# Kernel optimization log

Hardware: AMD Instinct MI355X
Metric: run time of the kernel (lower is better)

Reference implementation:

```python
import jax, jax.numpy as jnp
import numpy as np

N = 50000   # nodes
E = 800000  # edges
NF = 16     # num_node_features
EF = 8      # num_edge_features
H = 4       # heads
C = 64      # out_channels per head
NC = 4      # num_classes


def setup_inputs() -> dict:
    key = jax.random.key(0)
    ks = jax.random.split(key, 32)
    w = lambda k, shape: (jax.random.normal(k, shape, jnp.float32) * 0.05)
    inp = {
        "x": jax.random.normal(ks[0], (N, NF), jnp.float32),
        "edge_index": jax.random.randint(ks[1], (2, E), 0, N, dtype=jnp.int32),
        "edge_attr": jax.random.normal(ks[2], (E, EF), jnp.float32),
        # fc00
        "w00": w(ks[3], (NF, 64)), "b00": jnp.zeros((64,), jnp.float32),
        # edge MLP
        "we1": w(ks[4], (EF, 64)), "be1": jnp.zeros((64,), jnp.float32),
        "we2": w(ks[5], (64, 64)), "be2": jnp.zeros((64,), jnp.float32),
        "we3": w(ks[6], (64, 64)), "be3": jnp.zeros((64,), jnp.float32),
        # TransformerConv projections (64 -> H*C = 256)
        "wq": w(ks[7], (64, H * C)), "bq": jnp.zeros((H * C,), jnp.float32),
        "wk": w(ks[8], (64, H * C)), "bk": jnp.zeros((H * C,), jnp.float32),
        "wv": w(ks[9], (64, H * C)), "bv": jnp.zeros((H * C,), jnp.float32),
        "wedge": w(ks[10], (64, H * C)), "bedge": jnp.zeros((H * C,), jnp.float32),
        "wskip": w(ks[11], (64, H * C)), "bskip": jnp.zeros((H * C,), jnp.float32),
        # LayerNorm(256)
        "ln_g": jnp.ones((H * C,), jnp.float32), "ln_b": jnp.zeros((H * C,), jnp.float32),
        # head
        "w1": w(ks[12], (H * C, 128)), "b1": jnp.zeros((128,), jnp.float32),
        "w2": w(ks[13], (128, NC)), "b2": jnp.zeros((NC,), jnp.float32),
    }
    return inp


def _forward(x, edge_attr, w00, b00, we1, be1, we2, be2, we3, be3,
             wq, bq, wk, bk, wv, bv, wedge, bedge, wskip, bskip,
             ln_g, ln_b, w1, b1, w2, b2, edge_index):
    relu = jax.nn.relu
    n = x.shape[0]
    # node embed (dropout = identity in eval)
    x1 = relu(x @ w00 + b00)                              # [N, 64]
    # edge MLP
    e = relu(edge_attr @ we1 + be1)
    e = relu(e @ we2 + be2)
    e = relu(e @ we3 + be3)                               # [E, 64]
    src, dst = edge_index[0], edge_index[1]
    # project nodes once, then gather per edge
    q = (x1 @ wq + bq).reshape(n, H, C)[dst]              # [E, H, C]
    k = (x1 @ wk + bk).reshape(n, H, C)[src]
    v = (x1 @ wv + bv).reshape(n, H, C)[src]
    eh = (e @ wedge + bedge).reshape(-1, H, C)            # [E, H, C]
    k = k + eh
    v = v + eh
    alpha = jnp.sum(q * k, axis=-1) / np.sqrt(C)          # [E, H]
    # segment softmax over incoming edges of each target node
    m = jax.ops.segment_max(alpha, dst, num_segments=n)   # [N, H]
    m = jnp.where(jnp.isfinite(m), m, 0.0)
    p = jnp.exp(alpha - m[dst])
    s = jax.ops.segment_sum(p, dst, num_segments=n)
    a = p / (s[dst] + 1e-16)                              # [E, H]
    out = jax.ops.segment_sum(v * a[:, :, None], dst, num_segments=n)
    out = out.reshape(n, H * C) + (x1 @ wskip + bskip)    # root skip (root_weight=True)
    # LayerNorm(256)
    mu = jnp.mean(out, axis=-1, keepdims=True)
    var = jnp.mean(jnp.square(out - mu), axis=-1, keepdims=True)
    out = (out - mu) * jax.lax.rsqrt(var + 1e-5) * ln_g + ln_b
    out = relu(out)
    h = relu(out @ w1 + b1)
    logits = h @ w2 + b2
    return jax.nn.log_softmax(logits, axis=1)


def reference(x, edge_index, edge_attr, w00, b00, we1, be1, we2, be2, we3, be3,
              wq, bq, wk, bk, wv, bv, wedge, bedge, wskip, bskip,
              ln_g, ln_b, w1, b1, w2, b2):
    return _forward(x, edge_attr, w00, b00, we1, be1, we2, be2, we3, be3,
                    wq, bq, wk, bk, wv, bv, wedge, bedge, wskip, bskip,
                    ln_g, ln_b, w1, b1, w2, b2, edge_index)
```

## Files before the change

kernel.cpp:

```cpp
#include <hip/hip_runtime.h>
#include <hip/hip_bf16.h>

typedef unsigned short u16;
typedef __attribute__((ext_vector_type(8))) short bf16x8;
typedef __attribute__((ext_vector_type(4))) float f32x4;

#define NN 50000
#define NE 800000
#define SCAN_NB ((NN + 255) / 256)

__device__ __forceinline__ float bf2f(u16 u) { return __uint_as_float(((unsigned)u) << 16); }
__device__ __forceinline__ u16 f2bf(float f) {
  unsigned u = __float_as_uint(f);
  return (u16)((u + 0x7FFFu + ((u >> 16) & 1u)) >> 16);
}

__global__ void k_zero(int* __restrict__ deg) {
  int i = blockIdx.x * 256 + threadIdx.x;
  if (i < NN) deg[i] = 0;
}

__global__ void k_hist(const int* __restrict__ ei, int* __restrict__ deg) {
  int i = blockIdx.x * 256 + threadIdx.x;
  if (i < NE) {
    int d = ei[NE + i];
    if (d >= 0 && d < NN) atomicAdd(&deg[d], 1);
  }
}

__global__ __launch_bounds__(256) void k_scan_a(const int* __restrict__ deg,
                                                int* __restrict__ bsum) {
  __shared__ int red[256];
  const int t = threadIdx.x;
  const int i = blockIdx.x * 256 + t;
  red[t] = (i < NN) ? deg[i] : 0;
  __syncthreads();
  #pragma unroll
  for (int s = 128; s > 0; s >>= 1) {
    if (t < s) red[t] += red[t + s];
    __syncthreads();
  }
  if (t == 0) bsum[blockIdx.x] = red[0];
}

__global__ __launch_bounds__(256) void k_scan_b(const int* __restrict__ bsum,
                                                int* __restrict__ boff,
                                                int* __restrict__ rowptr) {
  __shared__ int s[256];
  const int t = threadIdx.x;
  int v = (t < SCAN_NB) ? bsum[t] : 0;
  s[t] = v;
  __syncthreads();
  #pragma unroll
  for (int o = 1; o < 256; o <<= 1) {
    int u = (t >= o) ? s[t - o] : 0;
    __syncthreads();
    s[t] += u;
    __syncthreads();
  }
  if (t < SCAN_NB) boff[t] = s[t] - v;
  if (t == 255) rowptr[NN] = s[255];
}

__global__ __launch_bounds__(256) void k_scan_c(const int* __restrict__ deg,
                                                const int* __restrict__ boff,
                                                int* __restrict__ rowptr,
                                                int* __restrict__ cursor) {
  __shared__ int s[256];
  const int t = threadIdx.x;
  const int i = blockIdx.x * 256 + t;
  int v = (i < NN) ? deg[i] : 0;
  s[t] = v;
  __syncthreads();
  #pragma unroll
  for (int o = 1; o < 256; o <<= 1) {
    int u = (t >= o) ? s[t - o] : 0;
    __syncthreads();
    s[t] += u;
    __syncthreads();
  }
  if (i < NN) {
    int r = boff[blockIdx.x] + s[t] - v;
    rowptr[i] = r;
    cursor[i] = r;
  }
}

__global__ void k_scatter(const int* __restrict__ ei, int* __restrict__ cursor,
                          int* __restrict__ slist, int* __restrict__ e2p) {
  int i = blockIdx.x * 256 + threadIdx.x;
  if (i < NE) {
    int d = ei[NE + i];
    if (d >= 0 && d < NN) {
      int pos = atomicAdd(&cursor[d], 1);
      if (pos >= 0 && pos < NE) {
        e2p[i] = pos;
        int s = ei[i];
        slist[pos] = max(0, min(s, NN - 1));
      }
    }
  }
}

__global__ void k_prep_ng(const float* __restrict__ w00, const float* __restrict__ wq,
                          const float* __restrict__ wedge, const float* __restrict__ wk,
                          u16* __restrict__ wB00t, u16* __restrict__ wqt, u16* __restrict__ BGQ) {
  int i = blockIdx.x * 256 + threadIdx.x;
  if (i < 2048) {
    int n = i >> 5, k = i & 31;
    wB00t[i] = (k < 16) ? f2bf(w00[k * 64 + n]) : (u16)0;
  } else if (i < 2048 + 16384) {
    int i2 = i - 2048;
    int n = i2 >> 6, k = i2 & 63;
    wqt[i2] = f2bf(wq[k * 256 + n]);
  } else if (i < 2048 + 16384 + 131072) {
    int i2 = i - 2048 - 16384;
    int col = i2 >> 8, k = i2 & 255;
    float v;
    if (col < 256) v = ((k >> 6) == (col >> 6)) ? wedge[(col & 63) * 256 + k] : 0.f;
    else { int c = col - 256; v = ((k >> 6) == (c >> 6)) ? wk[(c & 63) * 256 + k] : 0.f; }
    BGQ[i2] = f2bf(v);
  }
}

__global__ void k_prep_w(const float* __restrict__ we1, const float* __restrict__ we2,
                         const float* __restrict__ we3,
                         u16* __restrict__ wB1t, u16* __restrict__ wB2t, u16* __restrict__ wB3t) {
  int i = blockIdx.x * 256 + threadIdx.x;
  if (i < 512) {
    int n = i >> 3, k = i & 7;
    wB1t[i] = f2bf(we1[k * 64 + n]);
  } else if (i < 512 + 4096) {
    int i2 = i - 512;
    int n = i2 >> 6, k = i2 & 63;
    wB2t[i2] = f2bf(we2[k * 64 + n]);
  } else if (i < 512 + 8192) {
    int i2 = i - 512 - 4096;
    int n = i2 >> 6, k = i2 & 63;
    wB3t[i2] = f2bf(we3[k * 64 + n]);
  }
}

__global__ void k_prep_b(const float* __restrict__ wedge, const float* __restrict__ wv,
                         const float* __restrict__ wskip, u16* __restrict__ Bt) {
  const int col = blockIdx.x;
  const int k = threadIdx.x;
  float v;
  if (k < 256) v = ((k >> 6) == (col >> 6)) ? wedge[(k & 63) * 256 + col] : 0.f;
  else if (k < 512) { int k2 = k - 256; v = ((k2 >> 6) == (col >> 6)) ? wv[(k2 & 63) * 256 + col] : 0.f; }
  else v = wskip[(k - 512) * 256 + col];
  Bt[col * 576 + k] = f2bf(v);
}

__global__ void k_prep_h(const float* __restrict__ w1, u16* __restrict__ Bt1) {
  const int col = blockIdx.x;
  const int k = threadIdx.x;
  Bt1[col * 256 + k] = f2bf(w1[k * 128 + col]);
}

__global__ __launch_bounds__(256) void k_ng(
    const float* __restrict__ x, const u16* __restrict__ wB00t, const float* __restrict__ b00,
    const u16* __restrict__ wqt, const float* __restrict__ bq,
    const u16* __restrict__ BGQ,
    u16* __restrict__ x1g, u16* __restrict__ Gg, u16* __restrict__ Qkg) {
  __shared__ u16 xs[64 * 32];
  __shared__ u16 x1s[64 * 72];
  __shared__ u16 qs[64 * 264];
  const int t = threadIdx.x;
  const int w = t >> 6, l = t & 63;
  const int quad = l >> 4, li = l & 15;
  const int n0 = blockIdx.x * 64;
  const f32x4 zc = {0.f, 0.f, 0.f, 0.f};

  for (int q = t; q < 2048; q += 256) {
    int row = q >> 5, k = q & 31;
    float v = (k < 16 && n0 + row < NN) ? x[(size_t)(n0 + row) * 16 + k] : 0.f;
    xs[row * 32 + k] = f2bf(v);
  }
  __syncthreads();

  {
    bf16x8 bf = *(const bf16x8*)(wB00t + (w * 16 + li) * 32 + quad * 8);
    float bc = b00[w * 16 + li];
    #pragma unroll
    for (int mt = 0; mt < 4; ++mt) {
      bf16x8 af = *(const bf16x8*)(xs + (mt * 16 + li) * 32 + quad * 8);
      f32x4 d = __builtin_amdgcn_mfma_f32_16x16x32_bf16(af, bf, zc, 0, 0, 0);
      #pragma unroll
      for (int r = 0; r < 4; ++r)
        x1s[(mt * 16 + quad * 4 + r) * 72 + w * 16 + li] = f2bf(fmaxf(d[r] + bc, 0.f));
    }
  }
  __syncthreads();

  #pragma unroll
  for (int it = 0; it < 2; ++it) {
    int i = (it * 256 + t) * 8;
    int row = i >> 6, col = i & 63;
    if (n0 + row < NN)
      *(uint4*)(x1g + (size_t)(n0 + row) * 64 + col) = *(const uint4*)(x1s + row * 72 + col);
  }

  {
    f32x4 acc[4][4];
    #pragma unroll
    for (int mt = 0; mt < 4; ++mt)
      #pragma unroll
      for (int nt = 0; nt < 4; ++nt) acc[mt][nt] = zc;
    const int colbase = w * 64;
    #pragma unroll
    for (int s = 0; s < 2; ++s) {
      bf16x8 bf[4];
      #pragma unroll
      for (int nt = 0; nt < 4; ++nt)
        bf[nt] = *(const bf16x8*)(wqt + (size_t)(colbase + nt * 16 + li) * 64 + s * 32 + quad * 8);
      #pragma unroll
      for (int mt = 0; mt < 4; ++mt) {
        bf16x8 af = *(const bf16x8*)(x1s + (mt * 16 + li) * 72 + s * 32 + quad * 8);
        #pragma unroll
        for (int nt = 0; nt < 4; ++nt)
          acc[mt][nt] = __builtin_amdgcn_mfma_f32_16x16x32_bf16(af, bf[nt], acc[mt][nt], 0, 0, 0);
      }
    }
    float bqc[4];
    #pragma unroll
    for (int nt = 0; nt < 4; ++nt) bqc[nt] = bq[colbase + nt * 16 + li];
    #pragma unroll
    for (int mt = 0; mt < 4; ++mt)
      #pragma unroll
      for (int nt = 0; nt < 4; ++nt)
        #pragma unroll
        for (int r = 0; r < 4; ++r)
          qs[(mt * 16 + quad * 4 + r) * 264 + colbase + nt * 16 + li] = f2bf(acc[mt][nt][r] + bqc[nt]);
  }
  __syncthreads();

  #pragma unroll
  for (int half = 0; half < 2; ++half) {
    f32x4 acc[4][4];
    #pragma unroll
    for (int mt = 0; mt < 4; ++mt)
      #pragma unroll
      for (int nt = 0; nt < 4; ++nt) acc[mt][nt] = zc;
    const int colbase = w * 64;
    const size_t bofs = (size_t)(half * 256) * 256;
    #pragma unroll
    for (int s = 0; s < 8; ++s) {
      bf16x8 bf[4];
      #pragma unroll
      for (int nt = 0; nt < 4; ++nt)
        bf[nt] = *(const bf16x8*)(BGQ + bofs + (size_t)(colbase + nt * 16 + li) * 256 + s * 32 + quad * 8);
      #pragma unroll
      for (int mt = 0; mt < 4; ++mt) {
        bf16x8 af = *(const bf16x8*)(qs + (mt * 16 + li) * 264 + s * 32 + quad * 8);
        #pragma unroll
        for (int nt = 0; nt < 4; ++nt)
          acc[mt][nt] = __builtin_amdgcn_mfma_f32_16x16x32_bf16(af, bf[nt], acc[mt][nt], 0, 0, 0);
      }
    }
    u16* dst = half ? Qkg : Gg;
    #pragma unroll
    for (int mt = 0; mt < 4; ++mt)
      #pragma unroll
      for (int r = 0; r < 4; ++r) {
        int node = n0 + mt * 16 + quad * 4 + r;
        if (node < NN) {
          #pragma unroll
          for (int nt = 0; nt < 4; ++nt)
            dst[(size_t)node * 256 + colbase + nt * 16 + li] = f2bf(acc[mt][nt][r]);
        }
      }
  }
}

#define EPB 128
#define APAD 72
__global__ __launch_bounds__(256) void k_edge_mlp(
    const float* __restrict__ ea,
    const u16* __restrict__ wB1t, const u16* __restrict__ wB2t, const u16* __restrict__ wB3t,
    const float* __restrict__ be1, const float* __restrict__ be2, const float* __restrict__ be3,
    const int* __restrict__ e2p, u16* __restrict__ e3g) {
  __shared__ u16 actA[EPB * APAD];
  __shared__ u16 actB[EPB * APAD];
  const int t = threadIdx.x;
  const int w = t >> 6, l = t & 63;
  const int quad = l >> 4, li = l & 15;
  const int e0 = blockIdx.x * EPB;
  const f32x4 zc = {0.f, 0.f, 0.f, 0.f};

  float b1c[4], b2c[4], b3c[4];
  #pragma unroll
  for (int nt = 0; nt < 4; ++nt) {
    b1c[nt] = be1[nt * 16 + li];
    b2c[nt] = be2[nt * 16 + li];
    b3c[nt] = be3[nt * 16 + li];
  }

  bf16x8 b1f[4];
  #pragma unroll
  for (int nt = 0; nt < 4; ++nt) {
    bf16x8 z = {};
    if (quad == 0) z = *(const bf16x8*)(wB1t + (nt * 16 + li) * 8);
    b1f[nt] = z;
  }
  #pragma unroll
  for (int mi = 0; mi < 2; ++mi) {
    const int mt = w * 2 + mi;
    bf16x8 af = {};
    if (quad == 0) {
      const float4* pa = (const float4*)(ea + (size_t)(e0 + mt * 16 + li) * 8);
      float4 p0 = pa[0], p1 = pa[1];
      af[0] = (short)f2bf(p0.x); af[1] = (short)f2bf(p0.y);
      af[2] = (short)f2bf(p0.z); af[3] = (short)f2bf(p0.w);
      af[4] = (short)f2bf(p1.x); af[5] = (short)f2bf(p1.y);
      af[6] = (short)f2bf(p1.z); af[7] = (short)f2bf(p1.w);
    }
    #pragma unroll
    for (int nt = 0; nt < 4; ++nt) {
      f32x4 d = __builtin_amdgcn_mfma_f32_16x16x32_bf16(af, b1f[nt], zc, 0, 0, 0);
      #pragma unroll
      for (int r = 0; r < 4; ++r)
        actA[(mt * 16 + quad * 4 + r) * APAD + nt * 16 + li] = f2bf(fmaxf(d[r] + b1c[nt], 0.f));
    }
  }
  __syncthreads();

  {
    bf16x8 bf[4][2];
    #pragma unroll
    for (int nt = 0; nt < 4; ++nt)
      #pragma unroll
      for (int kk = 0; kk < 2; ++kk)
        bf[nt][kk] = *(const bf16x8*)(wB2t + (nt * 16 + li) * 64 + kk * 32 + quad * 8);
    #pragma unroll
    for (int mi = 0; mi < 2; ++mi) {
      const int mt = w * 2 + mi;
      bf16x8 a0 = *(const bf16x8*)(actA + (mt * 16 + li) * APAD + quad * 8);
      bf16x8 a1 = *(const bf16x8*)(actA + (mt * 16 + li) * APAD + 32 + quad * 8);
      #pragma unroll
      for (int nt = 0; nt < 4; ++nt) {
        f32x4 d = __builtin_amdgcn_mfma_f32_16x16x32_bf16(a0, bf[nt][0], zc, 0, 0, 0);
        d = __builtin_amdgcn_mfma_f32_16x16x32_bf16(a1, bf[nt][1], d, 0, 0, 0);
        #pragma unroll
        for (int r = 0; r < 4; ++r)
          actB[(mt * 16 + quad * 4 + r) * APAD + nt * 16 + li] = f2bf(fmaxf(d[r] + b2c[nt], 0.f));
      }
    }
  }
  __syncthreads();

  {
    bf16x8 bf[4][2];
    #pragma unroll
    for (int nt = 0; nt < 4; ++nt)
      #pragma unroll
      for (int kk = 0; kk < 2; ++kk)
        bf[nt][kk] = *(const bf16x8*)(wB3t + (nt * 16 + li) * 64 + kk * 32 + quad * 8);
    #pragma unroll
    for (int mi = 0; mi < 2; ++mi) {
      const int mt = w * 2 + mi;
      bf16x8 a0 = *(const bf16x8*)(actB + (mt * 16 + li) * APAD + quad * 8);
      bf16x8 a1 = *(const bf16x8*)(actB + (mt * 16 + li) * APAD + 32 + quad * 8);
      #pragma unroll
      for (int nt = 0; nt < 4; ++nt) {
        f32x4 d = __builtin_amdgcn_mfma_f32_16x16x32_bf16(a0, bf[nt][0], zc, 0, 0, 0);
        d = __builtin_amdgcn_mfma_f32_16x16x32_bf16(a1, bf[nt][1], d, 0, 0, 0);
        #pragma unroll
        for (int r = 0; r < 4; ++r)
          actA[(mt * 16 + quad * 4 + r) * APAD + nt * 16 + li] = f2bf(fmaxf(d[r] + b3c[nt], 0.f));
      }
    }
  }
  __syncthreads();

  #pragma unroll
  for (int it = 0; it < 4; ++it) {
    int flat = it * 2048 + t * 8;
    int el = flat >> 6, c = flat & 63;
    int pos = e2p[e0 + el];
    pos = ((unsigned)pos <= (unsigned)(NE - 1)) ? pos : NE;
    uint4 v = *(const uint4*)(actA + el * APAD + c);
    *(uint4*)(e3g + (size_t)pos * 64 + c) = v;
  }
}

__global__ __launch_bounds__(256) void k_attn(
    const int* __restrict__ rowptr, const int* __restrict__ slist,
    u16* yo, const u16* __restrict__ x1g, u16* gz, const u16* __restrict__ Qkg,
    const u16* __restrict__ e3g, float* __restrict__ bfac) {
  const int t = threadIdx.x;
  const int w = t >> 6;
  const int l = t & 63;
  const int grp = l >> 4;
  const int li = l & 15;
  const int chb = grp * 64 + li * 4;
  const int n = blockIdx.x * 4 + w;
  int base = rowptr[n];
  int end  = rowptr[n + 1];
  base = max(0, min(base, NE));
  end  = max(base, min(end, NE));
  if (l == 0) bfac[n] = (end > base) ? 1.f : 0.f;

  float Qkf[4], Gf[4];
  {
    ushort4 kv = *(const ushort4*)(Qkg + (size_t)n * 256 + chb);
    Qkf[0] = bf2f(kv.x); Qkf[1] = bf2f(kv.y); Qkf[2] = bf2f(kv.z); Qkf[3] = bf2f(kv.w);
    ushort4 gv = *(const ushort4*)(gz + (size_t)n * 256 + chb);
    Gf[0] = bf2f(gv.x); Gf[1] = bf2f(gv.y); Gf[2] = bf2f(gv.z); Gf[3] = bf2f(gv.w);
  }

  float s_run = 0.f;
  float y[4] = {0, 0, 0, 0}, zz[4] = {0, 0, 0, 0};
  int d = base;
  for (; d + 1 < end; d += 2) {
    int src0 = slist[d], src1 = slist[d + 1];
    src0 = max(0, min(src0, NN - 1)); src1 = max(0, min(src1, NN - 1));
    ushort4 x0 = *(const ushort4*)(x1g + (size_t)src0 * 64 + li * 4);
    ushort4 e0 = *(const ushort4*)(e3g + (size_t)d * 64 + li * 4);
    ushort4 x1v = *(const ushort4*)(x1g + (size_t)src1 * 64 + li * 4);
    ushort4 e1 = *(const ushort4*)(e3g + (size_t)(d + 1) * 64 + li * 4);
    float xf00 = bf2f(x0.x), xf01 = bf2f(x0.y), xf02 = bf2f(x0.z), xf03 = bf2f(x0.w);
    float ef00 = bf2f(e0.x), ef01 = bf2f(e0.y), ef02 = bf2f(e0.z), ef03 = bf2f(e0.w);
    float xf10 = bf2f(x1v.x), xf11 = bf2f(x1v.y), xf12 = bf2f(x1v.z), xf13 = bf2f(x1v.w);
    float ef10 = bf2f(e1.x), ef11 = bf2f(e1.y), ef12 = bf2f(e1.z), ef13 = bf2f(e1.w);
    float p0 = Qkf[0]*xf00 + Qkf[1]*xf01 + Qkf[2]*xf02 + Qkf[3]*xf03
             + Gf[0]*ef00 + Gf[1]*ef01 + Gf[2]*ef02 + Gf[3]*ef03;
    float p1 = Qkf[0]*xf10 + Qkf[1]*xf11 + Qkf[2]*xf12 + Qkf[3]*xf13
             + Gf[0]*ef10 + Gf[1]*ef11 + Gf[2]*ef12 + Gf[3]*ef13;
    #pragma unroll
    for (int mk = 1; mk < 16; mk <<= 1) { p0 += __shfl_xor(p0, mk); p1 += __shfl_xor(p1, mk); }
    float w0 = __expf(fminf(p0 * 0.125f, 60.f));
    float w1 = __expf(fminf(p1 * 0.125f, 60.f));
    s_run += w0 + w1;
    y[0] += w0*xf00 + w1*xf10; y[1] += w0*xf01 + w1*xf11;
    y[2] += w0*xf02 + w1*xf12; y[3] += w0*xf03 + w1*xf13;
    zz[0] += w0*ef00 + w1*ef10; zz[1] += w0*ef01 + w1*ef11;
    zz[2] += w0*ef02 + w1*ef12; zz[3] += w0*ef03 + w1*ef13;
  }
  if (d < end) {
    int src0 = slist[d];
    src0 = max(0, min(src0, NN - 1));
    ushort4 x0 = *(const ushort4*)(x1g + (size_t)src0 * 64 + li * 4);
    ushort4 e0 = *(const ushort4*)(e3g + (size_t)d * 64 + li * 4);
    float xf00 = bf2f(x0.x), xf01 = bf2f(x0.y), xf02 = bf2f(x0.z), xf03 = bf2f(x0.w);
    float ef00 = bf2f(e0.x), ef01 = bf2f(e0.y), ef02 = bf2f(e0.z), ef03 = bf2f(e0.w);
    float p0 = Qkf[0]*xf00 + Qkf[1]*xf01 + Qkf[2]*xf02 + Qkf[3]*xf03
             + Gf[0]*ef00 + Gf[1]*ef01 + Gf[2]*ef02 + Gf[3]*ef03;
    #pragma unroll
    for (int mk = 1; mk < 16; mk <<= 1) p0 += __shfl_xor(p0, mk);
    float w0 = __expf(fminf(p0 * 0.125f, 60.f));
    s_run += w0;
    y[0] += w0*xf00; y[1] += w0*xf01; y[2] += w0*xf02; y[3] += w0*xf03;
    zz[0] += w0*ef00; zz[1] += w0*ef01; zz[2] += w0*ef02; zz[3] += w0*ef03;
  }
  const float inv_s = 1.0f / (s_run + 1e-16f);
  ushort4 ynv, znv;
  ynv.x = f2bf(y[0] * inv_s); ynv.y = f2bf(y[1] * inv_s);
  ynv.z = f2bf(y[2] * inv_s); ynv.w = f2bf(y[3] * inv_s);
  znv.x = f2bf(zz[0] * inv_s); znv.y = f2bf(zz[1] * inv_s);
  znv.z = f2bf(zz[2] * inv_s); znv.w = f2bf(zz[3] * inv_s);
  *(ushort4*)(yo + (size_t)n * 256 + chb) = ynv;
  *(ushort4*)(gz + (size_t)n * 256 + chb) = znv;
}

#define PM 64
#define PK 576
#define PAPAD 584
__global__ __launch_bounds__(256) void k_post(
    const u16* __restrict__ zng, const u16* __restrict__ yng, const u16* __restrict__ x1g,
    const u16* __restrict__ Bt, const float* __restrict__ bfac,
    const float* __restrict__ bedge, const float* __restrict__ bv, const float* __restrict__ bskip,
    const float* __restrict__ lng, const float* __restrict__ lnb,
    u16* __restrict__ postg) {
  __shared__ u16 As[PM * PAPAD];
  __shared__ float ps1[PM * 4];
  __shared__ float ps2[PM * 4];
  const int t = threadIdx.x;
  const int w = t >> 6, l = t & 63;
  const int quad = l >> 4, li = l & 15;
  const int n0 = blockIdx.x * PM;

  for (int q = t; q < 2048; q += 256) {
    int row = q >> 5, off = (q & 31) * 8;
    uint4 vz = make_uint4(0, 0, 0, 0), vy = make_uint4(0, 0, 0, 0);
    if (n0 + row < NN) {
      vz = *(const uint4*)(zng + (size_t)(n0 + row) * 256 + off);
      vy = *(const uint4*)(yng + (size_t)(n0 + row) * 256 + off);
    }
    *(uint4*)(As + row * PAPAD + off) = vz;
    *(uint4*)(As + row * PAPAD + 256 + off) = vy;
  }
  for (int q = t; q < 512; q += 256) {
    int row = q >> 3, off = (q & 7) * 8;
    uint4 v = make_uint4(0, 0, 0, 0);
    if (n0 + row < NN) v = *(const uint4*)(x1g + (size_t)(n0 + row) * 64 + off);
    *(uint4*)(As + row * PAPAD + 512 + off) = v;
  }
  __syncthreads();

  f32x4 acc[4][4];
  #pragma unroll
  for (int mt = 0; mt < 4; ++mt)
    #pragma unroll
    for (int nt = 0; nt < 4; ++nt) acc[mt][nt] = (f32x4){0.f, 0.f, 0.f, 0.f};

  const int colbase = w * 64;
  #pragma unroll
  for (int s = 0; s < 18; ++s) {
    bf16x8 bf[4];
    #pragma unroll
    for (int nt = 0; nt < 4; ++nt)
      bf[nt] = *(const bf16x8*)(Bt + (size_t)(colbase + nt * 16 + li) * PK + s * 32 + quad * 8);
    #pragma unroll
    for (int mt = 0; mt < 4; ++mt) {
      bf16x8 af = *(const bf16x8*)(As + (mt * 16 + li) * PAPAD + s * 32 + quad * 8);
      #pragma unroll
      for (int nt = 0; nt < 4; ++nt)
        acc[mt][nt] = __builtin_amdgcn_mfma_f32_16x16x32_bf16(af, bf[nt], acc[mt][nt], 0, 0, 0);
    }
  }

  float beb[4], bs4[4], g4[4], lb4[4];
  #pragma unroll
  for (int nt = 0; nt < 4; ++nt) {
    int col = colbase + nt * 16 + li;
    beb[nt] = bedge[col] + bv[col];
    bs4[nt] = bskip[col]; g4[nt] = lng[col]; lb4[nt] = lnb[col];
  }
  #pragma unroll
  for (int mt = 0; mt < 4; ++mt) {
    #pragma unroll
    for (int r = 0; r < 4; ++r) {
      int node = n0 + mt * 16 + quad * 4 + r;
      float hasE = bfac[min(node, NN - 1)];
      #pragma unroll
      for (int nt = 0; nt < 4; ++nt)
        acc[mt][nt][r] += hasE * beb[nt] + bs4[nt];
    }
  }
  #pragma unroll
  for (int mt = 0; mt < 4; ++mt)
    #pragma unroll
    for (int r = 0; r < 4; ++r) {
      float s = acc[mt][0][r] + acc[mt][1][r] + acc[mt][2][r] + acc[mt][3][r];
      #pragma unroll
      for (int mk = 1; mk < 16; mk <<= 1) s += __shfl_xor(s, mk);
      if (li == 0) ps1[(mt * 16 + quad * 4 + r) * 4 + w] = s;
    }
  __syncthreads();
  float mu[4][4];
  #pragma unroll
  for (int mt = 0; mt < 4; ++mt)
    #pragma unroll
    for (int r = 0; r < 4; ++r) {
      float4 p = *(const float4*)(ps1 + (mt * 16 + quad * 4 + r) * 4);
      mu[mt][r] = (p.x + p.y + p.z + p.w) * (1.0f / 256.0f);
    }
  #pragma unroll
  for (int mt = 0; mt < 4; ++mt)
    #pragma unroll
    for (int r = 0; r < 4; ++r) {
      float m = mu[mt][r];
      float s = 0.f;
      #pragma unroll
      for (int nt = 0; nt < 4; ++nt) { float dd = acc[mt][nt][r] - m; s += dd * dd; }
      #pragma unroll
      for (int mk = 1; mk < 16; mk <<= 1) s += __shfl_xor(s, mk);
      if (li == 0) ps2[(mt * 16 + quad * 4 + r) * 4 + w] = s;
    }
  __syncthreads();
  #pragma unroll
  for (int mt = 0; mt < 4; ++mt)
    #pragma unroll
    for (int r = 0; r < 4; ++r) {
      float4 p = *(const float4*)(ps2 + (mt * 16 + quad * 4 + r) * 4);
      float rstd = rsqrtf((p.x + p.y + p.z + p.w) * (1.0f / 256.0f) + 1e-5f);
      int node = n0 + mt * 16 + quad * 4 + r;
      if (node < NN) {
        float m = mu[mt][r];
        #pragma unroll
        for (int nt = 0; nt < 4; ++nt) {
          int col = colbase + nt * 16 + li;
          postg[(size_t)node * 256 + col] =
              f2bf(fmaxf((acc[mt][nt][r] - m) * rstd * g4[nt] + lb4[nt], 0.f));
        }
      }
    }
}

#define HAPAD 264
#define H1PAD 136
__global__ __launch_bounds__(256) void k_head(
    const u16* __restrict__ postg, const u16* __restrict__ Bt1,
    const float* __restrict__ b1, const float* __restrict__ w2, const float* __restrict__ b2,
    float* __restrict__ outg) {
  __shared__ u16 As[64 * HAPAD];
  __shared__ u16 h1s[64 * H1PAD];
  const int t = threadIdx.x;
  const int w = t >> 6, l = t & 63;
  const int quad = l >> 4, li = l & 15;
  const int n0 = blockIdx.x * 64;

  for (int q = t; q < 2048; q += 256) {
    int row = q >> 5, off = (q & 31) * 8;
    uint4 v = make_uint4(0, 0, 0, 0);
    if (n0 + row < NN) v = *(const uint4*)(postg + (size_t)(n0 + row) * 256 + off);
    *(uint4*)(As + row * HAPAD + off) = v;
  }
  __syncthreads();

  f32x4 acc[4][2];
  #pragma unroll
  for (int mt = 0; mt < 4; ++mt)
    #pragma unroll
    for (int nt = 0; nt < 2; ++nt) acc[mt][nt] = (f32x4){0.f, 0.f, 0.f, 0.f};
  const int colbase = w * 32;
  #pragma unroll
  for (int s = 0; s < 8; ++s) {
    bf16x8 bf[2];
    #pragma unroll
    for (int nt = 0; nt < 2; ++nt)
      bf[nt] = *(const bf16x8*)(Bt1 + (size_t)(colbase + nt * 16 + li) * 256 + s * 32 + quad * 8);
    #pragma unroll
    for (int mt = 0; mt < 4; ++mt) {
      bf16x8 af = *(const bf16x8*)(As + (mt * 16 + li) * HAPAD + s * 32 + quad * 8);
      #pragma unroll
      for (int nt = 0; nt < 2; ++nt)
        acc[mt][nt] = __builtin_amdgcn_mfma_f32_16x16x32_bf16(af, bf[nt], acc[mt][nt], 0, 0, 0);
    }
  }
  float b1c[2];
  #pragma unroll
  for (int nt = 0; nt < 2; ++nt) b1c[nt] = b1[colbase + nt * 16 + li];
  #pragma unroll
  for (int mt = 0; mt < 4; ++mt)
    #pragma unroll
    for (int nt = 0; nt < 2; ++nt)
      #pragma unroll
      for (int r = 0; r < 4; ++r)
        h1s[(mt * 16 + quad * 4 + r) * H1PAD + colbase + nt * 16 + li] =
            f2bf(fmaxf(acc[mt][nt][r] + b1c[nt], 0.f));
  __syncthreads();

  const int node = t >> 2, c = t & 3;
  float lg = b2[c];
  const u16* hrow = h1s + node * H1PAD;
  #pragma unroll 4
  for (int j = 0; j < 128; ++j) lg += bf2f(hrow[j]) * w2[j * 4 + c];
  float mx = lg;
  #pragma unroll
  for (int mk = 1; mk < 4; mk <<= 1) mx = fmaxf(mx, __shfl_xor(mx, mk));
  float ex = __expf(lg - mx);
  float se = ex;
  #pragma unroll
  for (int mk = 1; mk < 4; mk <<= 1) se += __shfl_xor(se, mk);
  float res = lg - (mx + __logf(se));
  if (n0 + node < NN) outg[(size_t)(n0 + node) * 4 + c] = res;
}

extern "C" void kernel_launch(void* const* d_in, const int* in_sizes, int n_in,
                              void* d_out, int out_size, void* d_ws, size_t ws_size,
                              hipStream_t stream) {
  const float* x     = (const float*)d_in[0];
  const int*   ei    = (const int*)d_in[1];
  const float* ea    = (const float*)d_in[2];
  const float* w00   = (const float*)d_in[3];
  const float* b00   = (const float*)d_in[4];
  const float* we1   = (const float*)d_in[5];
  const float* be1   = (const float*)d_in[6];
  const float* we2   = (const float*)d_in[7];
  const float* be2   = (const float*)d_in[8];
  const float* we3   = (const float*)d_in[9];
  const float* be3   = (const float*)d_in[10];
  const float* wq    = (const float*)d_in[11];
  const float* bq    = (const float*)d_in[12];
  const float* wk    = (const float*)d_in[13];
  const float* bk    = (const float*)d_in[14];
  const float* wv    = (const float*)d_in[15];
  const float* bv    = (const float*)d_in[16];
  const float* wedge = (const float*)d_in[17];
  const float* bedge = (const float*)d_in[18];
  const float* wskip = (const float*)d_in[19];
  const float* bskip = (const float*)d_in[20];
  const float* lng   = (const float*)d_in[21];
  const float* lnb   = (const float*)d_in[22];
  const float* w1    = (const float*)d_in[23];
  const float* b1    = (const float*)d_in[24];
  const float* w2    = (const float*)d_in[25];
  const float* b2    = (const float*)d_in[26];
  float* outg = (float*)d_out;
  (void)bk;

  size_t off = 0;
  char* wsb = (char*)d_ws;
  auto carve = [&](size_t bytes) -> char* {
    char* r = wsb + off;
    off += (bytes + 255) & ~(size_t)255;
    return r;
  };
  u16* yg     = (u16*)carve((size_t)NN * 256 * 2);
  u16* Gg     = (u16*)carve((size_t)NN * 256 * 2);
  u16* Qkg    = (u16*)carve((size_t)NN * 256 * 2);
  u16* x1g    = (u16*)carve((size_t)NN * 64 * 2);
  u16* e3g    = (u16*)carve((size_t)(NE + 1) * 64 * 2);
  int* deg    = (int*)carve((size_t)NN * 4);
  int* rowptr = (int*)carve((size_t)(NN + 1) * 4);
  int* cursor = (int*)carve((size_t)NN * 4);
  int* slist  = (int*)carve((size_t)NE * 4);
  int* e2p    = (int*)carve((size_t)NE * 4);
  float* bfac = (float*)carve((size_t)NN * 4);
  int* bsum   = (int*)carve((size_t)SCAN_NB * 4);
  int* boff   = (int*)carve((size_t)SCAN_NB * 4);
  u16* wB00t  = (u16*)carve(2048 * 2);
  u16* wqt    = (u16*)carve(16384 * 2);
  u16* BGQ    = (u16*)carve((size_t)131072 * 2);
  u16* wB1t   = (u16*)carve(512 * 2);
  u16* wB2t   = (u16*)carve(4096 * 2);
  u16* wB3t   = (u16*)carve(4096 * 2);
  u16* Bt     = (u16*)carve((size_t)256 * 576 * 2);
  u16* Bt1    = (u16*)carve((size_t)128 * 256 * 2);
  u16* postg  = e3g;
  if (off > ws_size) return;

  k_prep_ng<<<584, 256, 0, stream>>>(w00, wq, wedge, wk, wB00t, wqt, BGQ);
  k_prep_w<<<34, 256, 0, stream>>>(we1, we2, we3, wB1t, wB2t, wB3t);
  k_prep_b<<<256, 576, 0, stream>>>(wedge, wv, wskip, Bt);
  k_prep_h<<<128, 256, 0, stream>>>(w1, Bt1);
  k_zero<<<SCAN_NB, 256, 0, stream>>>(deg);
  k_hist<<<NE / 256, 256, 0, stream>>>(ei, deg);
  k_scan_a<<<SCAN_NB, 256, 0, stream>>>(deg, bsum);
  k_scan_b<<<1, 256, 0, stream>>>(bsum, boff, rowptr);
  k_scan_c<<<SCAN_NB, 256, 0, stream>>>(deg, boff, rowptr, cursor);
  k_scatter<<<NE / 256, 256, 0, stream>>>(ei, cursor, slist, e2p);
  k_ng<<<(NN + 63) / 64, 256, 0, stream>>>(x, wB00t, b00, wqt, bq, BGQ, x1g, Gg, Qkg);
  k_edge_mlp<<<NE / EPB, 256, 0, stream>>>(ea, wB1t, wB2t, wB3t, be1, be2, be3, e2p, e3g);
  k_attn<<<NN / 4, 256, 0, stream>>>(rowptr, slist, yg, x1g, Gg, Qkg, e3g, bfac);
  k_post<<<(NN + PM - 1) / PM, 256, 0, stream>>>(Gg, yg, x1g, Bt, bfac, bedge, bv, bskip,
                                                 lng, lnb, postg);
  k_head<<<(NN + 63) / 64, 256, 0, stream>>>(postg, Bt1, b1, w2, b2, outg);
}
```

Before: 499.0 us.

## Merge prep kernels, unroll attention edge loop by 4, fuse post and head

```diff
diff --git a/kernel.cpp b/kernel.cpp
--- a/kernel.cpp
+++ b/kernel.cpp
@@ -13,11 +13,6 @@
 __device__ __forceinline__ u16 f2bf(float f) {
   unsigned u = __float_as_uint(f);
   return (u16)((u + 0x7FFFu + ((u >> 16) & 1u)) >> 16);
-}
-
-__global__ void k_zero(int* __restrict__ deg) {
-  int i = blockIdx.x * 256 + threadIdx.x;
-  if (i < NN) deg[i] = 0;
 }
 
 __global__ void k_hist(const int* __restrict__ ei, int* __restrict__ deg) {
@@ -102,60 +97,57 @@
   }
 }
 
-__global__ void k_prep_ng(const float* __restrict__ w00, const float* __restrict__ wq,
-                          const float* __restrict__ wedge, const float* __restrict__ wk,
-                          u16* __restrict__ wB00t, u16* __restrict__ wqt, u16* __restrict__ BGQ) {
+#define PREP_TOTAL 388432
+__global__ void k_prep_all(
+    const float* __restrict__ w00, const float* __restrict__ wq,
+    const float* __restrict__ wedge, const float* __restrict__ wk,
+    const float* __restrict__ we1, const float* __restrict__ we2, const float* __restrict__ we3,
+    const float* __restrict__ wv, const float* __restrict__ wskip, const float* __restrict__ w1,
+    u16* __restrict__ wB00t, u16* __restrict__ wqt, u16* __restrict__ BGQ,
+    u16* __restrict__ wB1t, u16* __restrict__ wB2t, u16* __restrict__ wB3t,
+    u16* __restrict__ Bt, u16* __restrict__ Bt1, int* __restrict__ deg) {
   int i = blockIdx.x * 256 + threadIdx.x;
   if (i < 2048) {
     int n = i >> 5, k = i & 31;
     wB00t[i] = (k < 16) ? f2bf(w00[k * 64 + n]) : (u16)0;
-  } else if (i < 2048 + 16384) {
+  } else if (i < 18432) {
     int i2 = i - 2048;
     int n = i2 >> 6, k = i2 & 63;
     wqt[i2] = f2bf(wq[k * 256 + n]);
-  } else if (i < 2048 + 16384 + 131072) {
-    int i2 = i - 2048 - 16384;
+  } else if (i < 149504) {
+    int i2 = i - 18432;
     int col = i2 >> 8, k = i2 & 255;
     float v;
     if (col < 256) v = ((k >> 6) == (col >> 6)) ? wedge[(col & 63) * 256 + k] : 0.f;
     else { int c = col - 256; v = ((k >> 6) == (c >> 6)) ? wk[(c & 63) * 256 + k] : 0.f; }
     BGQ[i2] = f2bf(v);
-  }
-}
-
-__global__ void k_prep_w(const float* __restrict__ we1, const float* __restrict__ we2,
-                         const float* __restrict__ we3,
-                         u16* __restrict__ wB1t, u16* __restrict__ wB2t, u16* __restrict__ wB3t) {
-  int i = blockIdx.x * 256 + threadIdx.x;
-  if (i < 512) {
-    int n = i >> 3, k = i & 7;
-    wB1t[i] = f2bf(we1[k * 64 + n]);
-  } else if (i < 512 + 4096) {
-    int i2 = i - 512;
+  } else if (i < 150016) {
+    int i2 = i - 149504;
+    int n = i2 >> 3, k = i2 & 7;
+    wB1t[i2] = f2bf(we1[k * 64 + n]);
+  } else if (i < 154112) {
+    int i2 = i - 150016;
     int n = i2 >> 6, k = i2 & 63;
     wB2t[i2] = f2bf(we2[k * 64 + n]);
-  } else if (i < 512 + 8192) {
-    int i2 = i - 512 - 4096;
+  } else if (i < 158208) {
+    int i2 = i - 154112;
     int n = i2 >> 6, k = i2 & 63;
     wB3t[i2] = f2bf(we3[k * 64 + n]);
-  }
-}
-
-__global__ void k_prep_b(const float* __restrict__ wedge, const float* __restrict__ wv,
-                         const float* __restrict__ wskip, u16* __restrict__ Bt) {
-  const int col = blockIdx.x;
-  const int k = threadIdx.x;
-  float v;
-  if (k < 256) v = ((k >> 6) == (col >> 6)) ? wedge[(k & 63) * 256 + col] : 0.f;
-  else if (k < 512) { int k2 = k - 256; v = ((k2 >> 6) == (col >> 6)) ? wv[(k2 & 63) * 256 + col] : 0.f; }
-  else v = wskip[(k - 512) * 256 + col];
-  Bt[col * 576 + k] = f2bf(v);
-}
-
-__global__ void k_prep_h(const float* __restrict__ w1, u16* __restrict__ Bt1) {
-  const int col = blockIdx.x;
-  const int k = threadIdx.x;
-  Bt1[col * 256 + k] = f2bf(w1[k * 128 + col]);
+  } else if (i < 305664) {
+    int i2 = i - 158208;
+    int col = i2 / 576, k = i2 - col * 576;
+    float v;
+    if (k < 256) v = ((k >> 6) == (col >> 6)) ? wedge[(k & 63) * 256 + col] : 0.f;
+    else if (k < 512) { int k2 = k - 256; v = ((k2 >> 6) == (col >> 6)) ? wv[(k2 & 63) * 256 + col] : 0.f; }
+    else v = wskip[(k - 512) * 256 + col];
+    Bt[i2] = f2bf(v);
+  } else if (i < 338432) {
+    int i2 = i - 305664;
+    int col = i2 >> 8, k = i2 & 255;
+    Bt1[i2] = f2bf(w1[k * 128 + col]);
+  } else if (i < PREP_TOTAL) {
+    deg[i - 338432] = 0;
+  }
 }
 
 __global__ __launch_bounds__(256) void k_ng(
@@ -412,32 +404,47 @@
   float s_run = 0.f;
   float y[4] = {0, 0, 0, 0}, zz[4] = {0, 0, 0, 0};
   int d = base;
-  for (; d + 1 < end; d += 2) {
-    int src0 = slist[d], src1 = slist[d + 1];
-    src0 = max(0, min(src0, NN - 1)); src1 = max(0, min(src1, NN - 1));
-    ushort4 x0 = *(const ushort4*)(x1g + (size_t)src0 * 64 + li * 4);
-    ushort4 e0 = *(const ushort4*)(e3g + (size_t)d * 64 + li * 4);
-    ushort4 x1v = *(const ushort4*)(x1g + (size_t)src1 * 64 + li * 4);
-    ushort4 e1 = *(const ushort4*)(e3g + (size_t)(d + 1) * 64 + li * 4);
-    float xf00 = bf2f(x0.x), xf01 = bf2f(x0.y), xf02 = bf2f(x0.z), xf03 = bf2f(x0.w);
-    float ef00 = bf2f(e0.x), ef01 = bf2f(e0.y), ef02 = bf2f(e0.z), ef03 = bf2f(e0.w);
-    float xf10 = bf2f(x1v.x), xf11 = bf2f(x1v.y), xf12 = bf2f(x1v.z), xf13 = bf2f(x1v.w);
-    float ef10 = bf2f(e1.x), ef11 = bf2f(e1.y), ef12 = bf2f(e1.z), ef13 = bf2f(e1.w);
-    float p0 = Qkf[0]*xf00 + Qkf[1]*xf01 + Qkf[2]*xf02 + Qkf[3]*xf03
-             + Gf[0]*ef00 + Gf[1]*ef01 + Gf[2]*ef02 + Gf[3]*ef03;
-    float p1 = Qkf[0]*xf10 + Qkf[1]*xf11 + Qkf[2]*xf12 + Qkf[3]*xf13
-             + Gf[0]*ef10 + Gf[1]*ef11 + Gf[2]*ef12 + Gf[3]*ef13;
-    #pragma unroll
-    for (int mk = 1; mk < 16; mk <<= 1) { p0 += __shfl_xor(p0, mk); p1 += __shfl_xor(p1, mk); }
-    float w0 = __expf(fminf(p0 * 0.125f, 60.f));
-    float w1 = __expf(fminf(p1 * 0.125f, 60.f));
-    s_run += w0 + w1;
-    y[0] += w0*xf00 + w1*xf10; y[1] += w0*xf01 + w1*xf11;
-    y[2] += w0*xf02 + w1*xf12; y[3] += w0*xf03 + w1*xf13;
-    zz[0] += w0*ef00 + w1*ef10; zz[1] += w0*ef01 + w1*ef11;
-    zz[2] += w0*ef02 + w1*ef12; zz[3] += w0*ef03 + w1*ef13;
-  }
-  if (d < end) {
+  for (; d + 3 < end; d += 4) {
+    int src[4];
+    #pragma unroll
+    for (int u = 0; u < 4; ++u) {
+      int s = slist[d + u];
+      src[u] = max(0, min(s, NN - 1));
+    }
+    ushort4 xv[4], ev[4];
+    #pragma unroll
+    for (int u = 0; u < 4; ++u) {
+      xv[u] = *(const ushort4*)(x1g + (size_t)src[u] * 64 + li * 4);
+      ev[u] = *(const ushort4*)(e3g + (size_t)(d + u) * 64 + li * 4);
+    }
+    float xf[4][4], ef[4][4], p[4];
+    #pragma unroll
+    for (int u = 0; u < 4; ++u) {
+      xf[u][0] = bf2f(xv[u].x); xf[u][1] = bf2f(xv[u].y);
+      xf[u][2] = bf2f(xv[u].z); xf[u][3] = bf2f(xv[u].w);
+      ef[u][0] = bf2f(ev[u].x); ef[u][1] = bf2f(ev[u].y);
+      ef[u][2] = bf2f(ev[u].z); ef[u][3] = bf2f(ev[u].w);
+      p[u] = Qkf[0]*xf[u][0] + Qkf[1]*xf[u][1] + Qkf[2]*xf[u][2] + Qkf[3]*xf[u][3]
+           + Gf[0]*ef[u][0] + Gf[1]*ef[u][1] + Gf[2]*ef[u][2] + Gf[3]*ef[u][3];
+    }
+    #pragma unroll
+    for (int mk = 1; mk < 16; mk <<= 1) {
+      p[0] += __shfl_xor(p[0], mk); p[1] += __shfl_xor(p[1], mk);
+      p[2] += __shfl_xor(p[2], mk); p[3] += __shfl_xor(p[3], mk);
+    }
+    float wt[4];
+    #pragma unroll
+    for (int u = 0; u < 4; ++u) wt[u] = __expf(fminf(p[u] * 0.125f, 60.f));
+    s_run += (wt[0] + wt[1]) + (wt[2] + wt[3]);
+    #pragma unroll
+    for (int u = 0; u < 4; ++u) {
+      y[0] += wt[u]*xf[u][0]; y[1] += wt[u]*xf[u][1];
+      y[2] += wt[u]*xf[u][2]; y[3] += wt[u]*xf[u][3];
+      zz[0] += wt[u]*ef[u][0]; zz[1] += wt[u]*ef[u][1];
+      zz[2] += wt[u]*ef[u][2]; zz[3] += wt[u]*ef[u][3];
+    }
+  }
+  for (; d < end; ++d) {
     int src0 = slist[d];
     src0 = max(0, min(src0, NN - 1));
     ushort4 x0 = *(const ushort4*)(x1g + (size_t)src0 * 64 + li * 4);
@@ -466,12 +473,16 @@
 #define PM 64
 #define PK 576
 #define PAPAD 584
-__global__ __launch_bounds__(256) void k_post(
+#define HAPAD 264
+#define H1PAD 136
+__global__ __launch_bounds__(256) void k_posthead(
     const u16* __restrict__ zng, const u16* __restrict__ yng, const u16* __restrict__ x1g,
     const u16* __restrict__ Bt, const float* __restrict__ bfac,
     const float* __restrict__ bedge, const float* __restrict__ bv, const float* __restrict__ bskip,
     const float* __restrict__ lng, const float* __restrict__ lnb,
-    u16* __restrict__ postg) {
+    const u16* __restrict__ Bt1, const float* __restrict__ b1,
+    const float* __restrict__ w2, const float* __restrict__ b2,
+    float* __restrict__ outg) {
   __shared__ u16 As[PM * PAPAD];
   __shared__ float ps1[PM * 4];
   __shared__ float ps2[PM * 4];
@@ -479,6 +490,7 @@
   const int w = t >> 6, l = t & 63;
   const int quad = l >> 4, li = l & 15;
   const int n0 = blockIdx.x * PM;
+  const f32x4 zc = {0.f, 0.f, 0.f, 0.f};
 
   for (int q = t; q < 2048; q += 256) {
     int row = q >> 5, off = (q & 31) * 8;
@@ -502,7 +514,7 @@
   #pragma unroll
   for (int mt = 0; mt < 4; ++mt)
     #pragma unroll
-    for (int nt = 0; nt < 4; ++nt) acc[mt][nt] = (f32x4){0.f, 0.f, 0.f, 0.f};
+    for (int nt = 0; nt < 4; ++nt) acc[mt][nt] = zc;
 
   const int colbase = w * 64;
   #pragma unroll
@@ -569,77 +581,58 @@
       if (li == 0) ps2[(mt * 16 + quad * 4 + r) * 4 + w] = s;
     }
   __syncthreads();
+  u16* postL = As;
+  u16* h1s   = As + 64 * HAPAD;
   #pragma unroll
   for (int mt = 0; mt < 4; ++mt)
     #pragma unroll
     for (int r = 0; r < 4; ++r) {
       float4 p = *(const float4*)(ps2 + (mt * 16 + quad * 4 + r) * 4);
       float rstd = rsqrtf((p.x + p.y + p.z + p.w) * (1.0f / 256.0f) + 1e-5f);
-      int node = n0 + mt * 16 + quad * 4 + r;
-      if (node < NN) {
-        float m = mu[mt][r];
+      float m = mu[mt][r];
+      int row = mt * 16 + quad * 4 + r;
+      #pragma unroll
+      for (int nt = 0; nt < 4; ++nt) {
+        int col = colbase + nt * 16 + li;
+        postL[row * HAPAD + col] =
+            f2bf(fmaxf((acc[mt][nt][r] - m) * rstd * g4[nt] + lb4[nt], 0.f));
+      }
+    }
+  __syncthreads();
+
+  {
+    f32x4 hacc[4][2];
+    #pragma unroll
+    for (int mt = 0; mt < 4; ++mt)
+      #pragma unroll
+      for (int nt = 0; nt < 2; ++nt) hacc[mt][nt] = zc;
+    const int hcb = w * 32;
+    #pragma unroll
+    for (int s = 0; s < 8; ++s) {
+      bf16x8 bf[2];
+      #pragma unroll
+      for (int nt = 0; nt < 2; ++nt)
+        bf[nt] = *(const bf16x8*)(Bt1 + (size_t)(hcb + nt * 16 + li) * 256 + s * 32 + quad * 8);
+      #pragma unroll
+      for (int mt = 0; mt < 4; ++mt) {
+        bf16x8 af = *(const bf16x8*)(postL + (mt * 16 + li) * HAPAD + s * 32 + quad * 8);
         #pragma unroll
-        for (int nt = 0; nt < 4; ++nt) {
-          int col = colbase + nt * 16 + li;
-          postg[(size_t)node * 256 + col] =
-              f2bf(fmaxf((acc[mt][nt][r] - m) * rstd * g4[nt] + lb4[nt], 0.f));
-        }
+        for (int nt = 0; nt < 2; ++nt)
+          hacc[mt][nt] = __builtin_amdgcn_mfma_f32_16x16x32_bf16(af, bf[nt], hacc[mt][nt], 0, 0, 0);
       }
     }
-}
-
-#define HAPAD 264
-#define H1PAD 136
-__global__ __launch_bounds__(256) void k_head(
-    const u16* __restrict__ postg, const u16* __restrict__ Bt1,
-    const float* __restrict__ b1, const float* __restrict__ w2, const float* __restrict__ b2,
-    float* __restrict__ outg) {
-  __shared__ u16 As[64 * HAPAD];
-  __shared__ u16 h1s[64 * H1PAD];
-  const int t = threadIdx.x;
-  const int w = t >> 6, l = t & 63;
-  const int quad = l >> 4, li = l & 15;
-  const int n0 = blockIdx.x * 64;
-
-  for (int q = t; q < 2048; q += 256) {
-    int row = q >> 5, off = (q & 31) * 8;
-    uint4 v = make_uint4(0, 0, 0, 0);
-    if (n0 + row < NN) v = *(const uint4*)(postg + (size_t)(n0 + row) * 256 + off);
-    *(uint4*)(As + row * HAPAD + off) = v;
-  }
-  __syncthreads();
-
-  f32x4 acc[4][2];
-  #pragma unroll
-  for (int mt = 0; mt < 4; ++mt)
-    #pragma unroll
-    for (int nt = 0; nt < 2; ++nt) acc[mt][nt] = (f32x4){0.f, 0.f, 0.f, 0.f};
-  const int colbase = w * 32;
-  #pragma unroll
-  for (int s = 0; s < 8; ++s) {
-    bf16x8 bf[2];
-    #pragma unroll
-    for (int nt = 0; nt < 2; ++nt)
-      bf[nt] = *(const bf16x8*)(Bt1 + (size_t)(colbase + nt * 16 + li) * 256 + s * 32 + quad * 8);
-    #pragma unroll
-    for (int mt = 0; mt < 4; ++mt) {
-      bf16x8 af = *(const bf16x8*)(As + (mt * 16 + li) * HAPAD + s * 32 + quad * 8);
+    float b1c[2];
+    #pragma unroll
+    for (int nt = 0; nt < 2; ++nt) b1c[nt] = b1[hcb + nt * 16 + li];
+    #pragma unroll
+    for (int mt = 0; mt < 4; ++mt)
       #pragma unroll
       for (int nt = 0; nt < 2; ++nt)
-        acc[mt][nt] = __builtin_amdgcn_mfma_f32_16x16x32_bf16(af, bf[nt], acc[mt][nt], 0, 0, 0);
-    }
-  }
-  float b1c[2];
-  #pragma unroll
-  for (int nt = 0; nt < 2; ++nt) b1c[nt] = b1[colbase + nt * 16 + li];
-  #pragma unroll
-  for (int mt = 0; mt < 4; ++mt)
-    #pragma unroll
-    for (int nt = 0; nt < 2; ++nt)
-      #pragma unroll
-      for (int r = 0; r < 4; ++r)
-        h1s[(mt * 16 + quad * 4 + r) * H1PAD + colbase + nt * 16 + li] =
-            f2bf(fmaxf(acc[mt][nt][r] + b1c[nt], 0.f));
+        #pragma unroll
+        for (int r = 0; r < 4; ++r)
+          h1s[(mt * 16 + quad * 4 + r) * H1PAD + hcb + nt * 16 + li] =
+              f2bf(fmaxf(hacc[mt][nt][r] + b1c[nt], 0.f));
+  }
   __syncthreads();
 
   const int node = t >> 2, c = t & 3;
@@ -719,14 +712,11 @@
   u16* wB3t   = (u16*)carve(4096 * 2);
   u16* Bt     = (u16*)carve((size_t)256 * 576 * 2);
   u16* Bt1    = (u16*)carve((size_t)128 * 256 * 2);
-  u16* postg  = e3g;
   if (off > ws_size) return;
 
-  k_prep_ng<<<584, 256, 0, stream>>>(w00, wq, wedge, wk, wB00t, wqt, BGQ);
-  k_prep_w<<<34, 256, 0, stream>>>(we1, we2, we3, wB1t, wB2t, wB3t);
-  k_prep_b<<<256, 576, 0, stream>>>(wedge, wv, wskip, Bt);
-  k_prep_h<<<128, 256, 0, stream>>>(w1, Bt1);
-  k_zero<<<SCAN_NB, 256, 0, stream>>>(deg);
+  k_prep_all<<<(PREP_TOTAL + 255) / 256, 256, 0, stream>>>(
+      w00, wq, wedge, wk, we1, we2, we3, wv, wskip, w1,
+      wB00t, wqt, BGQ, wB1t, wB2t, wB3t, Bt, Bt1, deg);
   k_hist<<<NE / 256, 256, 0, stream>>>(ei, deg);
   k_scan_a<<<SCAN_NB, 256, 0, stream>>>(deg, bsum);
   k_scan_b<<<1, 256, 0, stream>>>(bsum, boff, rowptr);
@@ -735,7 +725,6 @@
   k_ng<<<(NN + 63) / 64, 256, 0, stream>>>(x, wB00t, b00, wqt, bq, BGQ, x1g, Gg, Qkg);
   k_edge_mlp<<<NE / EPB, 256, 0, stream>>>(ea, wB1t, wB2t, wB3t, be1, be2, be3, e2p, e3g);
   k_attn<<<NN / 4, 256, 0, stream>>>(rowptr, slist, yg, x1g, Gg, Qkg, e3g, bfac);
-  k_post<<<(NN + PM - 1) / PM, 256, 0, stream>>>(Gg, yg, x1g, Bt, bfac, bedge, bv, bskip,
-                                                 lng, lnb, postg);
-  k_head<<<(NN + 63) / 64, 256, 0, stream>>>(postg, Bt1, b1, w2, b2, outg);
-}
+  k_posthead<<<(NN + PM - 1) / PM, 256, 0, stream>>>(
+      Gg, yg, x1g, Bt, bfac, bedge, bv, bskip, lng, lnb, Bt1, b1, w2, b2, outg);
+}
```

New measurement: 473.7 us. 1.05x faster.
